# Optimization experiments

Measured on AMD Instinct MI355X. Metric: run time of the kernel, lower is better.

The kernel has to match this reference:

```python
import jax, jax.numpy as jnp
import numpy as np

N, T, D, H = 256, 128, 64, 8  # spatial tokens, timesteps, per-head dim, heads


def setup_inputs() -> dict:
    key = jax.random.key(0)
    ks = jax.random.split(key, 8)
    s = 0.05
    return {
        "x": jax.random.normal(ks[0], (N, T, D), dtype=jnp.float32),
        "Wq": jax.random.normal(ks[1], (H * D, D), dtype=jnp.float32) * s,
        "bq": jax.random.normal(ks[2], (H * D,), dtype=jnp.float32) * s,
        "Wk": jax.random.normal(ks[3], (H * D, D), dtype=jnp.float32) * s,
        "bk": jax.random.normal(ks[4], (H * D,), dtype=jnp.float32) * s,
        "Wv": jax.random.normal(ks[5], (H * D, D), dtype=jnp.float32) * s,
        "bv": jax.random.normal(ks[6], (H * D,), dtype=jnp.float32) * s,
        "attention_weights": jax.random.uniform(ks[7], (T, H, N, N), dtype=jnp.float32),
    }


def reference(x, Wq, bq, Wk, bk, Wv, bv, attention_weights):
    n, t, d = x.shape
    h = Wq.shape[0] // d
    scale = 1.0 / np.sqrt(d).astype(np.float32)
    # projections: (N, T, H, D)
    q = (x @ Wq.T + bq).reshape(n, t, h, d)
    k = (x @ Wk.T + bk).reshape(n, t, h, d)
    v = (x @ Wv.T + bv).reshape(n, t, h, d)
    # attention over the spatial axis N, batched over (T, H): (T, H, N, N)
    att = jnp.einsum("nthd,mthd->thnm", q, k) * scale
    att = att * attention_weights
    att = jax.nn.softmax(att, axis=-1)
    # (T, H, N, D)
    out = jnp.einsum("thnm,mthd->thnd", att, v)
    # replicate torch's permute(1,2,0,3).contiguous().view(N, T, H*D):
    # (T,H,N,D) -> (H,N,T,D) contiguous, reinterpreted as (N, T, H*D)
    out = jnp.transpose(out, (1, 2, 0, 3)).reshape(n, t, h * d)
    return out
```

## Files before the change

kernel.cpp:

```cpp
#include <hip/hip_runtime.h>

#define NTOK 256
#define TT 128
#define DD 64
#define HH 8

typedef __bf16 bf16_t;
typedef bf16_t bf16x8 __attribute__((ext_vector_type(8)));
typedef bf16_t bf16x4 __attribute__((ext_vector_type(4)));
typedef float f32x4 __attribute__((ext_vector_type(4)));

__device__ __forceinline__ bf16x8 load_f32x8_as_bf16(const float* p) {
    float4 a = *reinterpret_cast<const float4*>(p);
    float4 b = *reinterpret_cast<const float4*>(p + 4);
    bf16x8 r;
    r[0] = (bf16_t)a.x; r[1] = (bf16_t)a.y; r[2] = (bf16_t)a.z; r[3] = (bf16_t)a.w;
    r[4] = (bf16_t)b.x; r[5] = (bf16_t)b.y; r[6] = (bf16_t)b.z; r[7] = (bf16_t)b.w;
    return r;
}

__device__ __forceinline__ int swz(int row, int stride, int colbyte) {
    return row * stride + (colbyte ^ ((row & 7) << 4));
}

__global__ __launch_bounds__(512, 2)
void fused_kernel(const float* __restrict__ x,
                  const float* __restrict__ Wq, const float* __restrict__ bq,
                  const float* __restrict__ Wk, const float* __restrict__ bk,
                  const float* __restrict__ Wv, const float* __restrict__ bv,
                  const float* __restrict__ aw, float* __restrict__ out) {
    __shared__ __align__(16) char k_s[256 * 128];
    __shared__ __align__(16) char vt_s[64 * 512];
    __shared__ __align__(16) char un[8][8192];

    const int t    = blockIdx.x >> 3;
    const int h    = blockIdx.x & 7;
    const int wave = threadIdx.x >> 6;
    const int lane = threadIdx.x & 63;
    const int l15  = lane & 15, quad = lane >> 4;

    bf16x8 ax[2][2];
#pragma unroll
    for (int mt = 0; mt < 2; ++mt) {
        int n = wave * 32 + mt * 16 + l15;
        const float* xp = x + ((size_t)n * TT + t) * DD;
#pragma unroll
        for (int kt = 0; kt < 2; ++kt)
            ax[mt][kt] = load_f32x8_as_bf16(xp + kt * 32 + quad * 8);
    }

    bf16x8 qf[2][2];

    {
        bf16x8 bw[4][2];
        float bias[4];
#pragma unroll
        for (int dt = 0; dt < 4; ++dt) {
            const float* wp = Wq + ((size_t)(h * DD + dt * 16 + l15)) * DD;
#pragma unroll
            for (int kt = 0; kt < 2; ++kt)
                bw[dt][kt] = load_f32x8_as_bf16(wp + kt * 32 + quad * 8);
            bias[dt] = bq[h * DD + dt * 16 + l15];
        }
        char* qs = un[wave];
#pragma unroll
        for (int mt = 0; mt < 2; ++mt) {
#pragma unroll
            for (int dt = 0; dt < 4; ++dt) {
                f32x4 acc = {0.f, 0.f, 0.f, 0.f};
#pragma unroll
                for (int kt = 0; kt < 2; ++kt)
                    acc = __builtin_amdgcn_mfma_f32_16x16x32_bf16(
                        ax[mt][kt], bw[dt][kt], acc, 0, 0, 0);
#pragma unroll
                for (int r = 0; r < 4; ++r) {
                    int lr = mt * 16 + quad * 4 + r;
                    *reinterpret_cast<bf16_t*>(qs + swz(lr, 128, (dt * 16 + l15) * 2)) =
                        (bf16_t)((acc[r] + bias[dt]) * 0.125f);
                }
            }
        }
#pragma unroll
        for (int it = 0; it < 2; ++it) {
            int lr = it * 16 + l15;
#pragma unroll
            for (int kt = 0; kt < 2; ++kt)
                qf[it][kt] = *reinterpret_cast<const bf16x8*>(
                    qs + swz(lr, 128, kt * 64 + quad * 16));
        }
    }

    {
        bf16x8 bw[4][2];
        float bias[4];
#pragma unroll
        for (int dt = 0; dt < 4; ++dt) {
            const float* wp = Wk + ((size_t)(h * DD + dt * 16 + l15)) * DD;
#pragma unroll
            for (int kt = 0; kt < 2; ++kt)
                bw[dt][kt] = load_f32x8_as_bf16(wp + kt * 32 + quad * 8);
            bias[dt] = bk[h * DD + dt * 16 + l15];
        }
#pragma unroll
        for (int mt = 0; mt < 2; ++mt) {
#pragma unroll
            for (int dt = 0; dt < 4; ++dt) {
                f32x4 acc = {0.f, 0.f, 0.f, 0.f};
#pragma unroll
                for (int kt = 0; kt < 2; ++kt)
                    acc = __builtin_amdgcn_mfma_f32_16x16x32_bf16(
                        ax[mt][kt], bw[dt][kt], acc, 0, 0, 0);
#pragma unroll
                for (int r = 0; r < 4; ++r) {
                    int n = wave * 32 + mt * 16 + quad * 4 + r;
                    *reinterpret_cast<bf16_t*>(k_s + swz(n, 128, (dt * 16 + l15) * 2)) =
                        (bf16_t)(acc[r] + bias[dt]);
                }
            }
        }
    }

    {
        bf16x8 bw[4][2];
#pragma unroll
        for (int dt = 0; dt < 4; ++dt) {
            const float* wp = Wv + ((size_t)(h * DD + dt * 16 + l15)) * DD;
#pragma unroll
            for (int kt = 0; kt < 2; ++kt)
                bw[dt][kt] = load_f32x8_as_bf16(wp + kt * 32 + quad * 8);
        }
        f32x4 bvv[4];
#pragma unroll
        for (int dt = 0; dt < 4; ++dt)
            bvv[dt] = *reinterpret_cast<const f32x4*>(bv + h * DD + dt * 16 + quad * 4);
#pragma unroll
        for (int dt = 0; dt < 4; ++dt) {
#pragma unroll
            for (int mt = 0; mt < 2; ++mt) {
                f32x4 acc = {0.f, 0.f, 0.f, 0.f};
#pragma unroll
                for (int kt = 0; kt < 2; ++kt)
                    acc = __builtin_amdgcn_mfma_f32_16x16x32_bf16(
                        bw[dt][kt], ax[mt][kt], acc, 0, 0, 0);
#pragma unroll
                for (int r = 0; r < 4; ++r) {
                    int d = dt * 16 + quad * 4 + r;
                    int cb = (wave * 32 + mt * 16 + l15) * 2;
                    *reinterpret_cast<bf16_t*>(vt_s + swz(d, 512, cb)) =
                        (bf16_t)(acc[r] + bvv[dt][r]);
                }
            }
        }
    }

    __syncthreads();

    const float* wp = aw + (size_t)blockIdx.x * ((size_t)NTOK * NTOK);

    for (int it = 0; it < 2; ++it) {
        const int q0 = wave * 32 + it * 16;
        const float* wrow = wp + (size_t)(q0 + l15) * NTOK + quad * 4;

        f32x4 w4v[16];
#pragma unroll
        for (int j = 0; j < 16; ++j)
            w4v[j] = *reinterpret_cast<const f32x4*>(wrow + j * 16);

        f32x4 s[16];
        float mx = -1e30f;
#pragma unroll
        for (int j = 0; j < 16; ++j) {
            f32x4 acc = {0.f, 0.f, 0.f, 0.f};
#pragma unroll
            for (int kt = 0; kt < 2; ++kt) {
                int kn = j * 16 + l15;
                bf16x8 kf = *reinterpret_cast<const bf16x8*>(
                    k_s + swz(kn, 128, kt * 64 + quad * 16));
                acc = __builtin_amdgcn_mfma_f32_16x16x32_bf16(kf, qf[it][kt], acc, 0, 0, 0);
            }
            acc *= w4v[j];
            s[j] = acc;
            mx = fmaxf(mx, fmaxf(fmaxf(acc[0], acc[1]), fmaxf(acc[2], acc[3])));
        }
        mx = fmaxf(mx, __shfl_xor(mx, 16, 64));
        mx = fmaxf(mx, __shfl_xor(mx, 32, 64));

        float sm = 0.f;
#pragma unroll
        for (int j = 0; j < 16; ++j) {
#pragma unroll
            for (int r = 0; r < 4; ++r) {
                float e = __expf(s[j][r] - mx);
                s[j][r] = e;
                sm += e;
            }
        }
        sm += __shfl_xor(sm, 16, 64);
        sm += __shfl_xor(sm, 32, 64);
        const float inv = 1.f / sm;

        char* ps = un[wave];
#pragma unroll
        for (int j = 0; j < 16; ++j) {
            bf16x4 pk;
#pragma unroll
            for (int r = 0; r < 4; ++r) pk[r] = (bf16_t)(s[j][r] * inv);
            *reinterpret_cast<bf16x4*>(ps + swz(l15, 512, j * 32 + quad * 8)) = pk;
        }

        f32x4 o[4];
#pragma unroll
        for (int dt = 0; dt < 4; ++dt) o[dt] = (f32x4){0.f, 0.f, 0.f, 0.f};
#pragma unroll
        for (int kt = 0; kt < 8; ++kt) {
            bf16x8 ap = *reinterpret_cast<const bf16x8*>(
                ps + swz(l15, 512, kt * 64 + quad * 16));
#pragma unroll
            for (int dt = 0; dt < 4; ++dt) {
                int d = dt * 16 + l15;
                bf16x8 bvf = *reinterpret_cast<const bf16x8*>(
                    vt_s + swz(d, 512, kt * 64 + quad * 16));
                o[dt] = __builtin_amdgcn_mfma_f32_16x16x32_bf16(ap, bvf, o[dt], 0, 0, 0);
            }
        }

        char* ost = un[wave];
#pragma unroll
        for (int dt = 0; dt < 4; ++dt) {
#pragma unroll
            for (int r = 0; r < 4; ++r) {
                int row = quad * 4 + r;
                *reinterpret_cast<float*>(ost + swz(row, 256, (dt * 16 + l15) * 4)) =
                    o[dt][r];
            }
        }
#pragma unroll
        for (int i = 0; i < 4; ++i) {
            int row = i * 4 + quad;
            f32x4 v = *reinterpret_cast<const f32x4*>(ost + swz(row, 256, l15 * 16));
            *reinterpret_cast<f32x4*>(
                out + (((size_t)h * NTOK + q0 + row) * TT + t) * DD + l15 * 4) = v;
        }
    }
}

extern "C" void kernel_launch(void* const* d_in, const int* in_sizes, int n_in,
                              void* d_out, int out_size, void* d_ws, size_t ws_size,
                              hipStream_t stream) {
    const float* x  = (const float*)d_in[0];
    const float* Wq = (const float*)d_in[1];
    const float* bq = (const float*)d_in[2];
    const float* Wk = (const float*)d_in[3];
    const float* bk = (const float*)d_in[4];
    const float* Wv = (const float*)d_in[5];
    const float* bv = (const float*)d_in[6];
    const float* aw = (const float*)d_in[7];
    float* out = (float*)d_out;

    fused_kernel<<<TT * HH, 512, 0, stream>>>(x, Wq, bq, Wk, bk, Wv, bv, aw, out);
}
```

Before: 435.2 us.

## Halve block to 4 waves, replace LDS staging with lane shuffles, prefetch weights

The block shrinks from 8 to 4 waves, and each wave now handles 64 query rows instead of 32. The per-wave LDS scratch used for Q, P and output staging is removed. Q and probability fragments are rearranged into MFMA operand layout with cross-lane shuffles, and the PV product is transposed so each lane writes output rows directly as float4. The attention-weight rows for the next iteration are prefetched before the barrier and during softmax, and s_setprio raises wave priority around the MFMA loops. Together this cuts LDS footprint (for occupancy) and LDS traffic, at the cost of higher register pressure from the larger per-wave tiles.

```diff
diff --git a/kernel.cpp b/kernel.cpp
--- a/kernel.cpp
+++ b/kernel.cpp
@@ -23,7 +23,22 @@
     return row * stride + (colbyte ^ ((row & 7) << 4));
 }
 
-__global__ __launch_bounds__(512, 2)
+__device__ __forceinline__ bf16x4 shfl8(bf16x4 v, int src) {
+    union { bf16x4 b; int u[2]; } a;
+    a.b = v;
+    a.u[0] = __shfl(a.u[0], src, 64);
+    a.u[1] = __shfl(a.u[1], src, 64);
+    return a.b;
+}
+
+__device__ __forceinline__ bf16x8 combine8(bf16x4 lo, bf16x4 hi) {
+    bf16x8 r;
+    r[0] = lo[0]; r[1] = lo[1]; r[2] = lo[2]; r[3] = lo[3];
+    r[4] = hi[0]; r[5] = hi[1]; r[6] = hi[2]; r[7] = hi[3];
+    return r;
+}
+
+__global__ __launch_bounds__(256, 2)
 void fused_kernel(const float* __restrict__ x,
                   const float* __restrict__ Wq, const float* __restrict__ bq,
                   const float* __restrict__ Wk, const float* __restrict__ bk,
@@ -31,7 +46,6 @@
                   const float* __restrict__ aw, float* __restrict__ out) {
     __shared__ __align__(16) char k_s[256 * 128];
     __shared__ __align__(16) char vt_s[64 * 512];
-    __shared__ __align__(16) char un[8][8192];
 
     const int t    = blockIdx.x >> 3;
     const int h    = blockIdx.x & 7;
@@ -39,32 +53,74 @@
     const int lane = threadIdx.x & 63;
     const int l15  = lane & 15, quad = lane >> 4;
 
-    bf16x8 ax[2][2];
-#pragma unroll
-    for (int mt = 0; mt < 2; ++mt) {
-        int n = wave * 32 + mt * 16 + l15;
+    const int src1 = ((2 * quad) & 3) * 16 + l15;
+    const int src2 = ((2 * quad + 1) & 3) * 16 + l15;
+    const bool lowq = (quad < 2);
+
+    bf16x8 ax[4][2];
+#pragma unroll
+    for (int mt = 0; mt < 4; ++mt) {
+        int n = wave * 64 + mt * 16 + l15;
         const float* xp = x + ((size_t)n * TT + t) * DD;
 #pragma unroll
         for (int kt = 0; kt < 2; ++kt)
             ax[mt][kt] = load_f32x8_as_bf16(xp + kt * 32 + quad * 8);
     }
 
-    bf16x8 qf[2][2];
+    bf16x8 qf[4][2];
+
+    {
+        bf16x8 bw[4][2];
+        f32x4 bqv[4];
+#pragma unroll
+        for (int dt = 0; dt < 4; ++dt) {
+            const float* wp = Wq + ((size_t)(h * DD + dt * 16 + l15)) * DD;
+#pragma unroll
+            for (int kt = 0; kt < 2; ++kt)
+                bw[dt][kt] = load_f32x8_as_bf16(wp + kt * 32 + quad * 8);
+            bqv[dt] = *reinterpret_cast<const f32x4*>(bq + h * DD + dt * 16 + quad * 4);
+        }
+        bf16x4 qpk[4][4];
+#pragma unroll
+        for (int mt = 0; mt < 4; ++mt) {
+#pragma unroll
+            for (int dt = 0; dt < 4; ++dt) {
+                f32x4 acc = {0.f, 0.f, 0.f, 0.f};
+#pragma unroll
+                for (int kt = 0; kt < 2; ++kt)
+                    acc = __builtin_amdgcn_mfma_f32_16x16x32_bf16(
+                        bw[dt][kt], ax[mt][kt], acc, 0, 0, 0);
+#pragma unroll
+                for (int r = 0; r < 4; ++r)
+                    qpk[mt][dt][r] = (bf16_t)((acc[r] + bqv[dt][r]) * 0.125f);
+            }
+        }
+#pragma unroll
+        for (int it = 0; it < 4; ++it) {
+#pragma unroll
+            for (int kt = 0; kt < 2; ++kt) {
+                bf16x4 ae = shfl8(qpk[it][2 * kt],     src1);
+                bf16x4 be = shfl8(qpk[it][2 * kt],     src2);
+                bf16x4 ce = shfl8(qpk[it][2 * kt + 1], src1);
+                bf16x4 de = shfl8(qpk[it][2 * kt + 1], src2);
+                qf[it][kt] = combine8(lowq ? ae : ce, lowq ? be : de);
+            }
+        }
+    }
 
     {
         bf16x8 bw[4][2];
         float bias[4];
 #pragma unroll
         for (int dt = 0; dt < 4; ++dt) {
-            const float* wp = Wq + ((size_t)(h * DD + dt * 16 + l15)) * DD;
+            const float* wp = Wk + ((size_t)(h * DD + dt * 16 + l15)) * DD;
 #pragma unroll
             for (int kt = 0; kt < 2; ++kt)
                 bw[dt][kt] = load_f32x8_as_bf16(wp + kt * 32 + quad * 8);
-            bias[dt] = bq[h * DD + dt * 16 + l15];
-        }
-        char* qs = un[wave];
-#pragma unroll
-        for (int mt = 0; mt < 2; ++mt) {
+            bias[dt] = bk[h * DD + dt * 16 + l15];
+        }
+#pragma unroll
+        for (int mt = 0; mt < 4; ++mt) {
 #pragma unroll
             for (int dt = 0; dt < 4; ++dt) {
                 f32x4 acc = {0.f, 0.f, 0.f, 0.f};
@@ -74,45 +130,7 @@
                         ax[mt][kt], bw[dt][kt], acc, 0, 0, 0);
 #pragma unroll
                 for (int r = 0; r < 4; ++r) {
-                    int lr = mt * 16 + quad * 4 + r;
-                    *reinterpret_cast<bf16_t*>(qs + swz(lr, 128, (dt * 16 + l15) * 2)) =
-                        (bf16_t)((acc[r] + bias[dt]) * 0.125f);
-                }
-            }
-        }
-#pragma unroll
-        for (int it = 0; it < 2; ++it) {
-            int lr = it * 16 + l15;
-#pragma unroll
-            for (int kt = 0; kt < 2; ++kt)
-                qf[it][kt] = *reinterpret_cast<const bf16x8*>(
-                    qs + swz(lr, 128, kt * 64 + quad * 16));
-        }
-    }
-
-    {
-        bf16x8 bw[4][2];
-        float bias[4];
-#pragma unroll
-        for (int dt = 0; dt < 4; ++dt) {
-            const float* wp = Wk + ((size_t)(h * DD + dt * 16 + l15)) * DD;
-#pragma unroll
-            for (int kt = 0; kt < 2; ++kt)
-                bw[dt][kt] = load_f32x8_as_bf16(wp + kt * 32 + quad * 8);
-            bias[dt] = bk[h * DD + dt * 16 + l15];
-        }
-#pragma unroll
-        for (int mt = 0; mt < 2; ++mt) {
-#pragma unroll
-            for (int dt = 0; dt < 4; ++dt) {
-                f32x4 acc = {0.f, 0.f, 0.f, 0.f};
-#pragma unroll
-                for (int kt = 0; kt < 2; ++kt)
-                    acc = __builtin_amdgcn_mfma_f32_16x16x32_bf16(
-                        ax[mt][kt], bw[dt][kt], acc, 0, 0, 0);
-#pragma unroll
-                for (int r = 0; r < 4; ++r) {
-                    int n = wave * 32 + mt * 16 + quad * 4 + r;
+                    int n = wave * 64 + mt * 16 + quad * 4 + r;
                     *reinterpret_cast<bf16_t*>(k_s + swz(n, 128, (dt * 16 + l15) * 2)) =
                         (bf16_t)(acc[r] + bias[dt]);
                 }
@@ -136,7 +154,7 @@
 #pragma unroll
         for (int dt = 0; dt < 4; ++dt) {
 #pragma unroll
-            for (int mt = 0; mt < 2; ++mt) {
+            for (int mt = 0; mt < 4; ++mt) {
                 f32x4 acc = {0.f, 0.f, 0.f, 0.f};
 #pragma unroll
                 for (int kt = 0; kt < 2; ++kt)
@@ -144,8 +162,8 @@
                         bw[dt][kt], ax[mt][kt], acc, 0, 0, 0);
 #pragma unroll
                 for (int r = 0; r < 4; ++r) {
-                    int d = dt * 16 + quad * 4 + r;
-                    int cb = (wave * 32 + mt * 16 + l15) * 2;
+                    int d  = dt * 16 + quad * 4 + r;
+                    int cb = (wave * 64 + mt * 16 + l15) * 2;
                     *reinterpret_cast<bf16_t*>(vt_s + swz(d, 512, cb)) =
                         (bf16_t)(acc[r] + bvv[dt][r]);
                 }
@@ -153,21 +171,24 @@
         }
     }
 
-    __syncthreads();
-
     const float* wp = aw + (size_t)blockIdx.x * ((size_t)NTOK * NTOK);
-
-    for (int it = 0; it < 2; ++it) {
-        const int q0 = wave * 32 + it * 16;
-        const float* wrow = wp + (size_t)(q0 + l15) * NTOK + quad * 4;
-
-        f32x4 w4v[16];
+    f32x4 w4v[16];
+    {
+        const float* wrow = wp + (size_t)(wave * 64 + l15) * NTOK + quad * 4;
 #pragma unroll
         for (int j = 0; j < 16; ++j)
             w4v[j] = *reinterpret_cast<const f32x4*>(wrow + j * 16);
+    }
+
+    __syncthreads();
+
+#pragma unroll
+    for (int it = 0; it < 4; ++it) {
+        const int q0 = wave * 64 + it * 16;
 
         f32x4 s[16];
         float mx = -1e30f;
+        __builtin_amdgcn_s_setprio(1);
 #pragma unroll
         for (int j = 0; j < 16; ++j) {
             f32x4 acc = {0.f, 0.f, 0.f, 0.f};
@@ -182,6 +203,15 @@
             s[j] = acc;
             mx = fmaxf(mx, fmaxf(fmaxf(acc[0], acc[1]), fmaxf(acc[2], acc[3])));
         }
+        __builtin_amdgcn_s_setprio(0);
+
+        if (it < 3) {
+            const float* wrow = wp + (size_t)(q0 + 16 + l15) * NTOK + quad * 4;
+#pragma unroll
+            for (int j = 0; j < 16; ++j)
+                w4v[j] = *reinterpret_cast<const f32x4*>(wrow + j * 16);
+        }
+
         mx = fmaxf(mx, __shfl_xor(mx, 16, 64));
         mx = fmaxf(mx, __shfl_xor(mx, 32, 64));
 
@@ -199,13 +229,12 @@
         sm += __shfl_xor(sm, 32, 64);
         const float inv = 1.f / sm;
 
-        char* ps = un[wave];
+        bf16x4 ppk[16];
 #pragma unroll
         for (int j = 0; j < 16; ++j) {
-            bf16x4 pk;
-#pragma unroll
-            for (int r = 0; r < 4; ++r) pk[r] = (bf16_t)(s[j][r] * inv);
-            *reinterpret_cast<bf16x4*>(ps + swz(l15, 512, j * 32 + quad * 8)) = pk;
+#pragma unroll
+            for (int r = 0; r < 4; ++r)
+                ppk[j][r] = (bf16_t)(s[j][r] * inv);
         }
 
         f32x4 o[4];
@@ -213,34 +242,25 @@
         for (int dt = 0; dt < 4; ++dt) o[dt] = (f32x4){0.f, 0.f, 0.f, 0.f};
 #pragma unroll
         for (int kt = 0; kt < 8; ++kt) {
-            bf16x8 ap = *reinterpret_cast<const bf16x8*>(
-                ps + swz(l15, 512, kt * 64 + quad * 16));
+            bf16x4 ae = shfl8(ppk[2 * kt],     src1);
+            bf16x4 be = shfl8(ppk[2 * kt],     src2);
+            bf16x4 ce = shfl8(ppk[2 * kt + 1], src1);
+            bf16x4 de = shfl8(ppk[2 * kt + 1], src2);
+            bf16x8 pf = combine8(lowq ? ae : ce, lowq ? be : de);
+            __builtin_amdgcn_s_setprio(1);
 #pragma unroll
             for (int dt = 0; dt < 4; ++dt) {
-                int d = dt * 16 + l15;
-                bf16x8 bvf = *reinterpret_cast<const bf16x8*>(
-                    vt_s + swz(d, 512, kt * 64 + quad * 16));
-                o[dt] = __builtin_amdgcn_mfma_f32_16x16x32_bf16(ap, bvf, o[dt], 0, 0, 0);
-            }
-        }
-
-        char* ost = un[wave];
-#pragma unroll
-        for (int dt = 0; dt < 4; ++dt) {
-#pragma unroll
-            for (int r = 0; r < 4; ++r) {
-                int row = quad * 4 + r;
-                *reinterpret_cast<float*>(ost + swz(row, 256, (dt * 16 + l15) * 4)) =
-                    o[dt][r];
-            }
-        }
-#pragma unroll
-        for (int i = 0; i < 4; ++i) {
-            int row = i * 4 + quad;
-            f32x4 v = *reinterpret_cast<const f32x4*>(ost + swz(row, 256, l15 * 16));
-            *reinterpret_cast<f32x4*>(
-                out + (((size_t)h * NTOK + q0 + row) * TT + t) * DD + l15 * 4) = v;
-        }
+                bf16x8 vf = *reinterpret_cast<const bf16x8*>(
+                    vt_s + swz(dt * 16 + l15, 512, kt * 64 + quad * 16));
+                o[dt] = __builtin_amdgcn_mfma_f32_16x16x32_bf16(vf, pf, o[dt], 0, 0, 0);
+            }
+            __builtin_amdgcn_s_setprio(0);
+        }
+
+        float* orow = out + (((size_t)h * NTOK + q0 + l15) * TT + t) * DD;
+#pragma unroll
+        for (int dt = 0; dt < 4; ++dt)
+            *reinterpret_cast<f32x4*>(orow + dt * 16 + quad * 4) = o[dt];
     }
 }
 
@@ -257,5 +277,5 @@
     const float* aw = (const float*)d_in[7];
     float* out = (float*)d_out;
 
-    fused_kernel<<<TT * HH, 512, 0, stream>>>(x, Wq, bq, Wk, bk, Wv, bv, aw, out);
-}
+    fused_kernel<<<TT * HH, 256, 0, stream>>>(x, Wq, bq, Wk, bk, Wv, bv, aw, out);
+}
```

New measurement: 412.9 us. 5.1% less time.
